# Optimization experiments

Measured on AMD Instinct MI355X. Metric: run time of the kernel, lower is better.

The kernel has to match this reference:

```python
import jax, jax.numpy as jnp
import numpy as np

NUM_CLASSES = 13
MIN_PTS = 50
CLUSTER_THRESHOLD = 0.3
MAX_CLUSTERS = 10
PROB_THRESH = 0.05


def _fps_indices(pts, valid, S):
    # Deterministic farthest-point sampling restricted to `valid` points.
    # Invalid points get min-distance -inf so they are never selected.
    neg = jnp.where(valid, 0.0, -jnp.inf)  # [N]
    start = jnp.argmax(valid)  # first valid point

    def d2_to(i):
        return jnp.sum((pts - pts[i]) ** 2, axis=-1)  # [N]

    mind = d2_to(start) + neg

    def step(mind, _):
        nxt = jnp.argmax(mind)
        mind = jnp.minimum(mind, d2_to(nxt) + neg)
        return mind, nxt

    _, rest = jax.lax.scan(step, mind, None, length=S - 1)
    return jnp.concatenate([start[None], rest])  # [S]


def _per_class(shifted, prob):
    # shifted: [N,3] shifted coords; prob: [N] softmax prob of this class.
    valid = prob > PROB_THRESH
    count = jnp.sum(valid)
    # num_seeds = min(max_clusters, count // min_pts, count); seeds k >= num_seeds are masked out
    num_seeds = jnp.minimum(jnp.minimum(MAX_CLUSTERS, count // MIN_PTS), count)
    idx = _fps_indices(shifted, valid, MAX_CLUSTERS)
    seeds = shifted[idx]  # [S,3]
    d2 = jnp.sum((shifted[:, None, :] - seeds[None, :, :]) ** 2, axis=-1)  # [N,S]
    sigma = CLUSTER_THRESHOLD * 0.5
    w = jnp.exp(-d2 / (2.0 * sigma * sigma))  # Gaussian soft ball query
    seed_valid = jnp.arange(MAX_CLUSTERS) < num_seeds  # [S]
    w = w * seed_valid[None, :].astype(w.dtype)
    assign = w / (jnp.sum(w, axis=-1, keepdims=True) + 1e-8)  # soft assignment over seeds
    # scatter into full mask == multiply by class prob gated by threshold membership
    final = assign * (prob * valid.astype(prob.dtype))[:, None]  # [N,S]
    return final.T, seed_valid  # [S,N], [S]


def _forward(semantic_logits, points, offsets):
    probs = jax.nn.softmax(semantic_logits, axis=-1)  # [B,N,C]
    shifted = points + offsets  # [B,N,3]
    per_class_all = jax.vmap(_per_class, in_axes=(None, 1))  # map over classes

    def per_batch(sh, pr):
        masks, seed_valid = per_class_all(sh, pr)  # [C,S,N], [C,S]
        K = NUM_CLASSES * MAX_CLUSTERS
        masks = masks.reshape(K, -1)  # [K,N]
        sv = seed_valid.reshape(K)
        # softmax(mask*10) over instance axis, restricted to valid instance rows
        logits = jnp.where(sv[:, None], masks * 10.0, -jnp.inf)
        out = jax.nn.softmax(logits, axis=0)
        return jnp.where(sv[:, None], out, 0.0)

    return jax.vmap(per_batch)(shifted, probs)  # [B, C*S, N]


def setup_inputs() -> dict:
    key = jax.random.key(0)
    k1, k2, k3 = jax.random.split(key, 3)
    B, N, C = 2, 65536, NUM_CLASSES
    semantic_logits = jax.random.normal(k1, (B, N, C), dtype=jnp.float32)
    points = jax.random.uniform(k2, (B, N, 3), dtype=jnp.float32)  # unit cube
    offsets = jax.random.normal(k3, (B, N, 3), dtype=jnp.float32) * 0.05  # small predicted shifts
    return {"semantic_logits": semantic_logits, "points": points, "offsets": offsets}


def reference(semantic_logits, points, offsets):
    return _forward(semantic_logits, points, offsets)
```

## Files before the change

### kernel.cpp

```cpp
#include <hip/hip_runtime.h>
#include <cstdint>

#define NCLS 13
#define SMAX 10
#define PTHRESH 0.05f
#define FPS_SEG 8
#define FPS_T 512
#define FPS_PPT 16
#define NSLOT 8
#define BCPAD 32
#define GABLK 256
#define BB 2
#define SLOT_DWORDS (BB * NCLS * SMAX * NSLOT * 2)

__device__ __forceinline__ float d2f(float ax, float ay, float az,
                                     float bx, float by, float bz) {
    float dx = ax - bx;
    float dy = ay - by;
    float dz = az - bz;
    return __fadd_rn(__fadd_rn(__fmul_rn(dx, dx), __fmul_rn(dy, dy)), __fmul_rn(dz, dz));
}

__device__ __forceinline__ unsigned int fmono(float f) {
    unsigned int u = __float_as_uint(f);
    return (u & 0x80000000u) ? ~u : (u | 0x80000000u);
}

__global__ void k_setup(const float* __restrict__ logits, const float* __restrict__ pts,
                        const float* __restrict__ offs, float* __restrict__ probs,
                        float4* __restrict__ xyzw, unsigned short* __restrict__ vmask,
                        unsigned int* __restrict__ pcnt, unsigned int* __restrict__ pfst,
                        unsigned int* __restrict__ slots32, int N) {
    int b = blockIdx.y;
    int n = blockIdx.x * blockDim.x + threadIdx.x;
    int t = threadIdx.x;
    __shared__ unsigned int sC[NCLS], sF[NCLS];
    if (t < NCLS) { sC[t] = 0u; sF[t] = 0xFFFFFFFFu; }
    __syncthreads();

    if (b == 0) {
        for (unsigned int i = blockIdx.x * blockDim.x + t; i < SLOT_DWORDS;
             i += GABLK * 256)
            slots32[i] = 0u;
    }

    if (n < N) {
        size_t bn = (size_t)b * N + n;
        const float* L = logits + bn * NCLS;
        float v[NCLS];
        float mx = -INFINITY;
#pragma unroll
        for (int c = 0; c < NCLS; ++c) { v[c] = L[c]; mx = fmaxf(mx, v[c]); }
        float s = 0.f;
#pragma unroll
        for (int c = 0; c < NCLS; ++c) { v[c] = expf(v[c] - mx); s += v[c]; }
        int lane = t & 63;
        int wave_base = n - lane;
        unsigned int msk = 0;
#pragma unroll
        for (int c = 0; c < NCLS; ++c) {
            float p = v[c] / s;
            probs[((size_t)b * NCLS + c) * N + n] = p;
            bool valid = p > PTHRESH;
            if (valid) msk |= (1u << c);
            unsigned long long m = __ballot(valid);
            if (lane == 0 && m) {
                atomicAdd(&sC[c], (unsigned int)__popcll(m));
                atomicMin(&sF[c], (unsigned int)(wave_base + __ffsll(m) - 1));
            }
        }
        float x = pts[bn * 3 + 0] + offs[bn * 3 + 0];
        float y = pts[bn * 3 + 1] + offs[bn * 3 + 1];
        float z = pts[bn * 3 + 2] + offs[bn * 3 + 2];
        xyzw[bn] = make_float4(x, y, z, 0.f);
        vmask[bn] = (unsigned short)msk;
    }
    __syncthreads();
    if (t < NCLS) {
        pcnt[(b * NCLS + t) * GABLK + blockIdx.x] = sC[t];
        pfst[(b * NCLS + t) * GABLK + blockIdx.x] = sF[t];
    }
}

__global__ __launch_bounds__(FPS_T, 1) void k_fps(
    const float4* __restrict__ xyzw, const unsigned short* __restrict__ vmask,
    const unsigned int* __restrict__ pcnt, const unsigned int* __restrict__ pfst,
    int* __restrict__ nseeds, float* __restrict__ seedxyz,
    unsigned long long* __restrict__ slots, int N) {
    int bid = blockIdx.x;
    int bc = bid & (BCPAD - 1);
    int g = bid >> 5;
    if (bc >= BB * NCLS) return;
    int b = bc / NCLS;
    int c = bc - b * NCLS;
    int t = threadIdx.x, lane = t & 63, w = t >> 6;

    const unsigned int* pc = pcnt + (size_t)bc * GABLK;
    const unsigned int* pf = pfst + (size_t)bc * GABLK;
    uint4 c4 = *(const uint4*)(pc + lane * 4);
    uint4 f4 = *(const uint4*)(pf + lane * 4);
    unsigned int cnt = c4.x + c4.y + c4.z + c4.w;
    unsigned int fst = min(min(f4.x, f4.y), min(f4.z, f4.w));
#pragma unroll
    for (int off = 1; off < 64; off <<= 1) {
        cnt += __shfl_xor(cnt, off, 64);
        fst = min(fst, __shfl_xor(fst, off, 64));
    }
    int ns = min(SMAX, min((int)cnt / 50, (int)cnt));
    if (g == 0 && t == 0) nseeds[bc] = ns;
    if (ns == 0) return;

    const float4* P4 = xyzw + (size_t)b * N;
    const unsigned short* VM = vmask + (size_t)b * N;

    int base = g * (FPS_T * FPS_PPT) + t;
    float X[FPS_PPT], Y[FPS_PPT], Z[FPS_PPT], m[FPS_PPT];
    unsigned int vm = 0;
#pragma unroll
    for (int j = 0; j < FPS_PPT; ++j) {
        int n = base + (j << 9);
        float4 q = P4[n];
        X[j] = q.x; Y[j] = q.y; Z[j] = q.z;
        if ((VM[n] >> c) & 1) vm |= (1u << j);
        m[j] = INFINITY;
    }

    int st = (int)fst;
    float4 q0 = P4[st];
    float cx = q0.x, cy = q0.y, cz = q0.z;
    if (g == 0 && t == 0) {
        float* sd = seedxyz + (size_t)bc * SMAX * 3;
        sd[0] = cx; sd[1] = cy; sd[2] = cz;
    }

    __shared__ unsigned long long s_keys[2][FPS_T / 64];

    for (int s = 1; s < ns; ++s) {
        float best = -INFINITY;
        int bidx = 0;
#pragma unroll
        for (int j = 0; j < FPS_PPT; ++j) {
            int n = base + (j << 9);
            float d2 = d2f(X[j], Y[j], Z[j], cx, cy, cz);
            float add = ((vm >> j) & 1u) ? 0.0f : -INFINITY;
            float nm = fminf(m[j], __fadd_rn(d2, add));
            m[j] = nm;
            if (nm > best) { best = nm; bidx = n; }
        }
        unsigned long long key =
            ((unsigned long long)fmono(best) << 32) | (unsigned int)(~(unsigned int)bidx);
#pragma unroll
        for (int off = 1; off < 64; off <<= 1) {
            unsigned long long ok = __shfl_xor(key, off, 64);
            if (ok > key) key = ok;
        }
        int par = s & 1;
        if (lane == 0) s_keys[par][w] = key;
        __syncthreads();

        unsigned long long* sl = slots + ((size_t)bc * SMAX + s) * NSLOT;
        if (w == 0) {
            unsigned long long bk = (lane < 8) ? s_keys[par][lane] : 0ULL;
#pragma unroll
            for (int off = 1; off < 8; off <<= 1) {
                unsigned long long ok = __shfl_xor(bk, off, 8);
                if (ok > bk) bk = ok;
            }
            if (lane == 0)
                __hip_atomic_store(&sl[g], bk, __ATOMIC_RELAXED, __HIP_MEMORY_SCOPE_AGENT);
        }
        asm volatile("" ::: "memory");
        unsigned long long kk = 0ULL;
        while (true) {
            if (lane < NSLOT && kk == 0ULL)
                kk = __hip_atomic_load(&sl[lane], __ATOMIC_RELAXED,
                                       __HIP_MEMORY_SCOPE_AGENT);
            if (__all(kk != 0ULL || lane >= NSLOT)) break;
        }
        asm volatile("" ::: "memory");
#pragma unroll
        for (int off = 1; off < 8; off <<= 1) {
            unsigned long long ok = __shfl_xor(kk, off, 8);
            if (ok > kk) kk = ok;
        }
        kk = __shfl(kk, 0, 64);

        int widx = (int)(~(unsigned int)kk);
        float4 qw = P4[widx];
        cx = qw.x; cy = qw.y; cz = qw.z;
        if (g == 0 && t == 0) {
            float* sd = seedxyz + ((size_t)bc * SMAX + s) * 3;
            sd[0] = cx; sd[1] = cy; sd[2] = cz;
        }
    }
}

__global__ __launch_bounds__(512) void k_out(
    const float* __restrict__ probs, const float4* __restrict__ xyzw,
    const int* __restrict__ nseeds, const float* __restrict__ seedxyz,
    float* __restrict__ out, int N) {
    int b = blockIdx.y;
    int t = threadIdx.x;
    int lane = t & 63;
    int wv = t >> 6;
    int n0 = blockIdx.x * 128 + lane * 2;

    __shared__ float S[NCLS * SMAX * 3];
    __shared__ int NSs[NCLS];
    __shared__ float gdS[NCLS][128];
    __shared__ float psum[8][128];
    if (t < NCLS * SMAX * 3) S[t] = seedxyz[(size_t)b * NCLS * SMAX * 3 + t];
    if (t >= 448 && t < 448 + NCLS) NSs[t - 448] = nseeds[b * NCLS + (t - 448)];
    __syncthreads();

    float4 q0 = xyzw[(size_t)b * N + n0];
    float4 q1 = xyzw[(size_t)b * N + n0 + 1];

    const float kinv = 22.2222222f;
    float ps0 = 0.f, ps1 = 0.f;
#pragma unroll
    for (int c = wv; c < NCLS; c += 8) {
        int ns = NSs[c];
        float gdv0 = 0.f, gdv1 = 0.f;
        if (ns > 0) {
            float2 pv = *(const float2*)(probs + ((size_t)b * NCLS + c) * N + n0);
            if (pv.x > PTHRESH) {
                float wb[SMAX]; float sw = 0.f;
#pragma unroll
                for (int s = 0; s < SMAX; ++s) {
                    wb[s] = 0.f;
                    if (s < ns) {
                        const float* sd = &S[(c * SMAX + s) * 3];
                        float d2 = d2f(q0.x, q0.y, q0.z, sd[0], sd[1], sd[2]);
                        wb[s] = __expf(-d2 * kinv);
                        sw += wb[s];
                    }
                }
                gdv0 = __fdividef(pv.x, sw + 1e-8f);
#pragma unroll
                for (int s = 0; s < SMAX; ++s)
                    if (s < ns) ps0 += __expf(10.f * wb[s] * gdv0);
            } else {
                ps0 += (float)ns;
            }
            if (pv.y > PTHRESH) {
                float wb[SMAX]; float sw = 0.f;
#pragma unroll
                for (int s = 0; s < SMAX; ++s) {
                    wb[s] = 0.f;
                    if (s < ns) {
                        const float* sd = &S[(c * SMAX + s) * 3];
                        float d2 = d2f(q1.x, q1.y, q1.z, sd[0], sd[1], sd[2]);
                        wb[s] = __expf(-d2 * kinv);
                        sw += wb[s];
                    }
                }
                gdv1 = __fdividef(pv.y, sw + 1e-8f);
#pragma unroll
                for (int s = 0; s < SMAX; ++s)
                    if (s < ns) ps1 += __expf(10.f * wb[s] * gdv1);
            } else {
                ps1 += (float)ns;
            }
        }
        gdS[c][lane * 2] = gdv0;
        gdS[c][lane * 2 + 1] = gdv1;
    }
    psum[wv][lane * 2] = ps0;
    psum[wv][lane * 2 + 1] = ps1;
    __syncthreads();

    float tot0 = 0.f, tot1 = 0.f;
#pragma unroll
    for (int w = 0; w < 8; ++w) {
        tot0 += psum[w][lane * 2];
        tot1 += psum[w][lane * 2 + 1];
    }
    float inv0 = __fdividef(1.f, tot0);
    float inv1 = __fdividef(1.f, tot1);

    float* ob = out + (size_t)b * (NCLS * SMAX) * N + n0;
#pragma unroll
    for (int k = 0; k < NCLS * SMAX; k += 8) {
        int kk = k + wv;
        if (kk >= NCLS * SMAX) break;
        int c = kk / SMAX, s = kk - c * SMAX;
        float o0 = 0.f, o1 = 0.f;
        if (s < NSs[c]) {
            float g0 = gdS[c][lane * 2];
            float g1 = gdS[c][lane * 2 + 1];
            const float* sd = &S[(c * SMAX + s) * 3];
            if (g0 > 0.f) {
                float d2 = d2f(q0.x, q0.y, q0.z, sd[0], sd[1], sd[2]);
                o0 = __expf(10.f * __expf(-d2 * kinv) * g0) * inv0;
            } else {
                o0 = inv0;
            }
            if (g1 > 0.f) {
                float d2 = d2f(q1.x, q1.y, q1.z, sd[0], sd[1], sd[2]);
                o1 = __expf(10.f * __expf(-d2 * kinv) * g1) * inv1;
            } else {
                o1 = inv1;
            }
        }
        float2 st; st.x = o0; st.y = o1;
        *(float2*)(ob + (size_t)kk * N) = st;
    }
}

extern "C" void kernel_launch(void* const* d_in, const int* in_sizes, int n_in,
                              void* d_out, int out_size, void* d_ws, size_t ws_size,
                              hipStream_t stream) {
    const float* logits = (const float*)d_in[0];
    const float* pts    = (const float*)d_in[1];
    const float* offs   = (const float*)d_in[2];
    float* out = (float*)d_out;

    const int B = BB;
    const int BN = in_sizes[0] / NCLS;
    const int N = BN / B;

    char* w = (char*)d_ws;
    size_t off = 0;
    auto take = [&](size_t bytes) -> void* {
        void* p = w + off;
        off = (off + bytes + 255) & ~(size_t)255;
        return p;
    };
    float* probs   = (float*)take((size_t)B * NCLS * N * sizeof(float));
    float4* xyzw   = (float4*)take((size_t)B * N * sizeof(float4));
    unsigned short* vmsk = (unsigned short*)take((size_t)B * N * sizeof(unsigned short));
    float* seedxyz = (float*)take((size_t)B * NCLS * SMAX * 3 * sizeof(float));
    unsigned int* pcnt = (unsigned int*)take((size_t)B * NCLS * GABLK * sizeof(unsigned int));
    unsigned int* pfst = (unsigned int*)take((size_t)B * NCLS * GABLK * sizeof(unsigned int));
    int* nseeds        = (int*)take(B * NCLS * sizeof(int));
    unsigned long long* slots =
        (unsigned long long*)take((size_t)B * NCLS * SMAX * NSLOT * sizeof(unsigned long long));

    dim3 gA((N + 255) / 256, B);
    k_setup<<<gA, 256, 0, stream>>>(logits, pts, offs, probs, xyzw, vmsk,
                                    pcnt, pfst, (unsigned int*)slots, N);

    k_fps<<<BCPAD * FPS_SEG, FPS_T, 0, stream>>>(xyzw, vmsk, pcnt, pfst,
                                                 nseeds, seedxyz, slots, N);

    dim3 gC(N / 128, B);
    k_out<<<gC, 512, 0, stream>>>(probs, xyzw, nseeds, seedxyz, out, N);
}
```

Before: 64.16 us.

## Cache per-seed exponentials in LDS and process one point per thread

The output kernel now stores each seed's softmax numerator in a shared-memory table during the first pass and reads it back in the write pass. Before, the distance and two exponentials were computed a second time there. Blocks shrink to 256 threads with one point per thread instead of two, and the grid doubles. The trade-off is about 33KB of LDS per block, which may limit occupancy, and output stores are now scalar rather than float2.

```diff
diff --git a/kernel.cpp b/kernel.cpp
--- a/kernel.cpp
+++ b/kernel.cpp
@@ -11,6 +11,7 @@
 #define BCPAD 32
 #define GABLK 256
 #define BB 2
+#define OUT_T 256
 #define SLOT_DWORDS (BB * NCLS * SMAX * NSLOT * 2)
 
 __device__ __forceinline__ float d2f(float ax, float ay, float az,
@@ -195,7 +196,7 @@
     }
 }
 
-__global__ __launch_bounds__(512) void k_out(
+__global__ __launch_bounds__(OUT_T) void k_out(
     const float* __restrict__ probs, const float4* __restrict__ xyzw,
     const int* __restrict__ nseeds, const float* __restrict__ seedxyz,
     float* __restrict__ out, int N) {
@@ -203,108 +204,69 @@
     int t = threadIdx.x;
     int lane = t & 63;
     int wv = t >> 6;
-    int n0 = blockIdx.x * 128 + lane * 2;
+    int n = blockIdx.x * 64 + lane;
 
     __shared__ float S[NCLS * SMAX * 3];
     __shared__ int NSs[NCLS];
-    __shared__ float gdS[NCLS][128];
-    __shared__ float psum[8][128];
-    if (t < NCLS * SMAX * 3) S[t] = seedxyz[(size_t)b * NCLS * SMAX * 3 + t];
-    if (t >= 448 && t < 448 + NCLS) NSs[t - 448] = nseeds[b * NCLS + (t - 448)];
+    __shared__ float gdS[NCLS][64];
+    __shared__ float psum[4][64];
+    __shared__ float E[NCLS * SMAX][64];
+    for (int i = t; i < NCLS * SMAX * 3; i += OUT_T)
+        S[i] = seedxyz[(size_t)b * NCLS * SMAX * 3 + i];
+    if (t < NCLS) NSs[t] = nseeds[b * NCLS + t];
     __syncthreads();
 
-    float4 q0 = xyzw[(size_t)b * N + n0];
-    float4 q1 = xyzw[(size_t)b * N + n0 + 1];
+    float4 q = xyzw[(size_t)b * N + n];
 
     const float kinv = 22.2222222f;
-    float ps0 = 0.f, ps1 = 0.f;
-#pragma unroll
-    for (int c = wv; c < NCLS; c += 8) {
+    float ps = 0.f;
+    for (int c = wv; c < NCLS; c += 4) {
         int ns = NSs[c];
-        float gdv0 = 0.f, gdv1 = 0.f;
+        float gdv = 0.f;
         if (ns > 0) {
-            float2 pv = *(const float2*)(probs + ((size_t)b * NCLS + c) * N + n0);
-            if (pv.x > PTHRESH) {
-                float wb[SMAX]; float sw = 0.f;
+            float pv = probs[((size_t)b * NCLS + c) * N + n];
+            if (pv > PTHRESH) {
+                float wb[SMAX];
+                float sw = 0.f;
 #pragma unroll
                 for (int s = 0; s < SMAX; ++s) {
                     wb[s] = 0.f;
                     if (s < ns) {
                         const float* sd = &S[(c * SMAX + s) * 3];
-                        float d2 = d2f(q0.x, q0.y, q0.z, sd[0], sd[1], sd[2]);
+                        float d2 = d2f(q.x, q.y, q.z, sd[0], sd[1], sd[2]);
                         wb[s] = __expf(-d2 * kinv);
                         sw += wb[s];
                     }
                 }
-                gdv0 = __fdividef(pv.x, sw + 1e-8f);
+                gdv = __fdividef(pv, sw + 1e-8f);
 #pragma unroll
                 for (int s = 0; s < SMAX; ++s)
-                    if (s < ns) ps0 += __expf(10.f * wb[s] * gdv0);
+                    if (s < ns) {
+                        float e = __expf(10.f * wb[s] * gdv);
+                        E[c * SMAX + s][lane] = e;
+                        ps += e;
+                    }
             } else {
-                ps0 += (float)ns;
+                ps += (float)ns;
             }
-            if (pv.y > PTHRESH) {
-                float wb[SMAX]; float sw = 0.f;
-#pragma unroll
-                for (int s = 0; s < SMAX; ++s) {
-                    wb[s] = 0.f;
-                    if (s < ns) {
-                        const float* sd = &S[(c * SMAX + s) * 3];
-                        float d2 = d2f(q1.x, q1.y, q1.z, sd[0], sd[1], sd[2]);
-                        wb[s] = __expf(-d2 * kinv);
-                        sw += wb[s];
-                    }
-                }
-                gdv1 = __fdividef(pv.y, sw + 1e-8f);
-#pragma unroll
-                for (int s = 0; s < SMAX; ++s)
-                    if (s < ns) ps1 += __expf(10.f * wb[s] * gdv1);
-            } else {
-                ps1 += (float)ns;
-            }
-        }
-        gdS[c][lane * 2] = gdv0;
-        gdS[c][lane * 2 + 1] = gdv1;
-    }
-    psum[wv][lane * 2] = ps0;
-    psum[wv][lane * 2 + 1] = ps1;
+        }
+        gdS[c][lane] = gdv;
+    }
+    psum[wv][lane] = ps;
     __syncthreads();
 
-    float tot0 = 0.f, tot1 = 0.f;
-#pragma unroll
-    for (int w = 0; w < 8; ++w) {
-        tot0 += psum[w][lane * 2];
-        tot1 += psum[w][lane * 2 + 1];
-    }
-    float inv0 = __fdividef(1.f, tot0);
-    float inv1 = __fdividef(1.f, tot1);
-
-    float* ob = out + (size_t)b * (NCLS * SMAX) * N + n0;
-#pragma unroll
-    for (int k = 0; k < NCLS * SMAX; k += 8) {
-        int kk = k + wv;
-        if (kk >= NCLS * SMAX) break;
+    float tot = psum[0][lane] + psum[1][lane] + psum[2][lane] + psum[3][lane];
+    float inv = __fdividef(1.f, tot);
+
+    float* ob = out + (size_t)b * (NCLS * SMAX) * N + n;
+    for (int kk = wv; kk < NCLS * SMAX; kk += 4) {
         int c = kk / SMAX, s = kk - c * SMAX;
-        float o0 = 0.f, o1 = 0.f;
+        float o = 0.f;
         if (s < NSs[c]) {
-            float g0 = gdS[c][lane * 2];
-            float g1 = gdS[c][lane * 2 + 1];
-            const float* sd = &S[(c * SMAX + s) * 3];
-            if (g0 > 0.f) {
-                float d2 = d2f(q0.x, q0.y, q0.z, sd[0], sd[1], sd[2]);
-                o0 = __expf(10.f * __expf(-d2 * kinv) * g0) * inv0;
-            } else {
-                o0 = inv0;
-            }
-            if (g1 > 0.f) {
-                float d2 = d2f(q1.x, q1.y, q1.z, sd[0], sd[1], sd[2]);
-                o1 = __expf(10.f * __expf(-d2 * kinv) * g1) * inv1;
-            } else {
-                o1 = inv1;
-            }
-        }
-        float2 st; st.x = o0; st.y = o1;
-        *(float2*)(ob + (size_t)kk * N) = st;
+            float gdv = gdS[c][lane];
+            o = (gdv > 0.f) ? E[kk][lane] * inv : inv;
+        }
+        ob[(size_t)kk * N] = o;
     }
 }
 
@@ -344,6 +306,6 @@
     k_fps<<<BCPAD * FPS_SEG, FPS_T, 0, stream>>>(xyzw, vmsk, pcnt, pfst,
                                                  nseeds, seedxyz, slots, N);
 
-    dim3 gC(N / 128, B);
-    k_out<<<gC, 512, 0, stream>>>(probs, xyzw, nseeds, seedxyz, out, N);
-}
+    dim3 gC(N / 64, B);
+    k_out<<<gC, OUT_T, 0, stream>>>(probs, xyzw, nseeds, seedxyz, out, N);
+}
```

Result: slower. 69.13 us (+7.7%).

## Recompute softmax in output kernel and cache exp terms in shared memory

Applied to the files above, without the earlier changes.

Stops writing the class-major probability buffer in the setup kernel. The output kernel now reloads the logits, recomputes the softmax per point, and uses the saved validity bitmask instead of a probability threshold test. It also stores every per-seed exponential in a large shared array, so the final write pass only scales by the inverse sum instead of recomputing distances and two exps. This cuts global traffic and duplicated transcendental work, but it raises shared memory use per block (about 66KB), which may lower occupancy, and it re-reads the logits through strided per-point loads.

```diff
diff --git a/kernel.cpp b/kernel.cpp
--- a/kernel.cpp
+++ b/kernel.cpp
@@ -11,6 +11,7 @@
 #define BCPAD 32
 #define GABLK 256
 #define BB 2
+#define OUT_T 512
 #define SLOT_DWORDS (BB * NCLS * SMAX * NSLOT * 2)
 
 __device__ __forceinline__ float d2f(float ax, float ay, float az,
@@ -27,7 +28,7 @@
 }
 
 __global__ void k_setup(const float* __restrict__ logits, const float* __restrict__ pts,
-                        const float* __restrict__ offs, float* __restrict__ probs,
+                        const float* __restrict__ offs,
                         float4* __restrict__ xyzw, unsigned short* __restrict__ vmask,
                         unsigned int* __restrict__ pcnt, unsigned int* __restrict__ pfst,
                         unsigned int* __restrict__ slots32, int N) {
@@ -60,7 +61,6 @@
 #pragma unroll
         for (int c = 0; c < NCLS; ++c) {
             float p = v[c] / s;
-            probs[((size_t)b * NCLS + c) * N + n] = p;
             bool valid = p > PTHRESH;
             if (valid) msk |= (1u << c);
             unsigned long long m = __ballot(valid);
@@ -195,8 +195,9 @@
     }
 }
 
-__global__ __launch_bounds__(512) void k_out(
-    const float* __restrict__ probs, const float4* __restrict__ xyzw,
+__global__ __launch_bounds__(OUT_T) void k_out(
+    const float* __restrict__ logits, const float4* __restrict__ xyzw,
+    const unsigned short* __restrict__ vmask,
     const int* __restrict__ nseeds, const float* __restrict__ seedxyz,
     float* __restrict__ out, int N) {
     int b = blockIdx.y;
@@ -204,107 +205,121 @@
     int lane = t & 63;
     int wv = t >> 6;
     int n0 = blockIdx.x * 128 + lane * 2;
+    int l2 = lane * 2;
 
     __shared__ float S[NCLS * SMAX * 3];
     __shared__ int NSs[NCLS];
-    __shared__ float gdS[NCLS][128];
     __shared__ float psum[8][128];
+    __shared__ float E[NCLS * SMAX][128];
     if (t < NCLS * SMAX * 3) S[t] = seedxyz[(size_t)b * NCLS * SMAX * 3 + t];
     if (t >= 448 && t < 448 + NCLS) NSs[t - 448] = nseeds[b * NCLS + (t - 448)];
     __syncthreads();
 
-    float4 q0 = xyzw[(size_t)b * N + n0];
-    float4 q1 = xyzw[(size_t)b * N + n0 + 1];
+    size_t bn0 = (size_t)b * N + n0;
+    float4 q0 = xyzw[bn0];
+    float4 q1 = xyzw[bn0 + 1];
+    unsigned int vm0 = vmask[bn0];
+    unsigned int vm1 = vmask[bn0 + 1];
+
+    const float* L0 = logits + bn0 * NCLS;
+    const float* L1 = L0 + NCLS;
+    float mx0 = -INFINITY, mx1 = -INFINITY;
+#pragma unroll
+    for (int c = 0; c < NCLS; ++c) {
+        mx0 = fmaxf(mx0, L0[c]);
+        mx1 = fmaxf(mx1, L1[c]);
+    }
+    float dn0 = 0.f, dn1 = 0.f;
+#pragma unroll
+    for (int c = 0; c < NCLS; ++c) {
+        dn0 += __expf(L0[c] - mx0);
+        dn1 += __expf(L1[c] - mx1);
+    }
+    float rd0 = __fdividef(1.f, dn0);
+    float rd1 = __fdividef(1.f, dn1);
 
     const float kinv = 22.2222222f;
     float ps0 = 0.f, ps1 = 0.f;
-#pragma unroll
     for (int c = wv; c < NCLS; c += 8) {
         int ns = NSs[c];
-        float gdv0 = 0.f, gdv1 = 0.f;
-        if (ns > 0) {
-            float2 pv = *(const float2*)(probs + ((size_t)b * NCLS + c) * N + n0);
-            if (pv.x > PTHRESH) {
-                float wb[SMAX]; float sw = 0.f;
-#pragma unroll
-                for (int s = 0; s < SMAX; ++s) {
-                    wb[s] = 0.f;
-                    if (s < ns) {
-                        const float* sd = &S[(c * SMAX + s) * 3];
-                        float d2 = d2f(q0.x, q0.y, q0.z, sd[0], sd[1], sd[2]);
-                        wb[s] = __expf(-d2 * kinv);
-                        sw += wb[s];
-                    }
+        if (ns == 0) continue;
+        if ((vm0 >> c) & 1) {
+            float pv = __expf(L0[c] - mx0) * rd0;
+            float wb[SMAX]; float sw = 0.f;
+#pragma unroll
+            for (int s = 0; s < SMAX; ++s) {
+                wb[s] = 0.f;
+                if (s < ns) {
+                    const float* sd = &S[(c * SMAX + s) * 3];
+                    float d2 = d2f(q0.x, q0.y, q0.z, sd[0], sd[1], sd[2]);
+                    wb[s] = __expf(-d2 * kinv);
+                    sw += wb[s];
                 }
-                gdv0 = __fdividef(pv.x, sw + 1e-8f);
-#pragma unroll
-                for (int s = 0; s < SMAX; ++s)
-                    if (s < ns) ps0 += __expf(10.f * wb[s] * gdv0);
-            } else {
-                ps0 += (float)ns;
             }
-            if (pv.y > PTHRESH) {
-                float wb[SMAX]; float sw = 0.f;
-#pragma unroll
-                for (int s = 0; s < SMAX; ++s) {
-                    wb[s] = 0.f;
-                    if (s < ns) {
-                        const float* sd = &S[(c * SMAX + s) * 3];
-                        float d2 = d2f(q1.x, q1.y, q1.z, sd[0], sd[1], sd[2]);
-                        wb[s] = __expf(-d2 * kinv);
-                        sw += wb[s];
-                    }
+            float gd = __fdividef(pv, sw + 1e-8f);
+#pragma unroll
+            for (int s = 0; s < SMAX; ++s)
+                if (s < ns) {
+                    float e = __expf(10.f * wb[s] * gd);
+                    E[c * SMAX + s][l2] = e;
+                    ps0 += e;
                 }
-                gdv1 = __fdividef(pv.y, sw + 1e-8f);
-#pragma unroll
-                for (int s = 0; s < SMAX; ++s)
-                    if (s < ns) ps1 += __expf(10.f * wb[s] * gdv1);
-            } else {
-                ps1 += (float)ns;
+        } else {
+#pragma unroll
+            for (int s = 0; s < SMAX; ++s)
+                if (s < ns) E[c * SMAX + s][l2] = 1.0f;
+            ps0 += (float)ns;
+        }
+        if ((vm1 >> c) & 1) {
+            float pv = __expf(L1[c] - mx1) * rd1;
+            float wb[SMAX]; float sw = 0.f;
+#pragma unroll
+            for (int s = 0; s < SMAX; ++s) {
+                wb[s] = 0.f;
+                if (s < ns) {
+                    const float* sd = &S[(c * SMAX + s) * 3];
+                    float d2 = d2f(q1.x, q1.y, q1.z, sd[0], sd[1], sd[2]);
+                    wb[s] = __expf(-d2 * kinv);
+                    sw += wb[s];
+                }
             }
-        }
-        gdS[c][lane * 2] = gdv0;
-        gdS[c][lane * 2 + 1] = gdv1;
-    }
-    psum[wv][lane * 2] = ps0;
-    psum[wv][lane * 2 + 1] = ps1;
+            float gd = __fdividef(pv, sw + 1e-8f);
+#pragma unroll
+            for (int s = 0; s < SMAX; ++s)
+                if (s < ns) {
+                    float e = __expf(10.f * wb[s] * gd);
+                    E[c * SMAX + s][l2 + 1] = e;
+                    ps1 += e;
+                }
+        } else {
+#pragma unroll
+            for (int s = 0; s < SMAX; ++s)
+                if (s < ns) E[c * SMAX + s][l2 + 1] = 1.0f;
+            ps1 += (float)ns;
+        }
+    }
+    psum[wv][l2] = ps0;
+    psum[wv][l2 + 1] = ps1;
     __syncthreads();
 
     float tot0 = 0.f, tot1 = 0.f;
 #pragma unroll
     for (int w = 0; w < 8; ++w) {
-        tot0 += psum[w][lane * 2];
-        tot1 += psum[w][lane * 2 + 1];
+        tot0 += psum[w][l2];
+        tot1 += psum[w][l2 + 1];
     }
     float inv0 = __fdividef(1.f, tot0);
     float inv1 = __fdividef(1.f, tot1);
 
     float* ob = out + (size_t)b * (NCLS * SMAX) * N + n0;
-#pragma unroll
-    for (int k = 0; k < NCLS * SMAX; k += 8) {
-        int kk = k + wv;
-        if (kk >= NCLS * SMAX) break;
+    for (int kk = wv; kk < NCLS * SMAX; kk += 8) {
         int c = kk / SMAX, s = kk - c * SMAX;
-        float o0 = 0.f, o1 = 0.f;
+        float2 o; o.x = 0.f; o.y = 0.f;
         if (s < NSs[c]) {
-            float g0 = gdS[c][lane * 2];
-            float g1 = gdS[c][lane * 2 + 1];
-            const float* sd = &S[(c * SMAX + s) * 3];
-            if (g0 > 0.f) {
-                float d2 = d2f(q0.x, q0.y, q0.z, sd[0], sd[1], sd[2]);
-                o0 = __expf(10.f * __expf(-d2 * kinv) * g0) * inv0;
-            } else {
-                o0 = inv0;
-            }
-            if (g1 > 0.f) {
-                float d2 = d2f(q1.x, q1.y, q1.z, sd[0], sd[1], sd[2]);
-                o1 = __expf(10.f * __expf(-d2 * kinv) * g1) * inv1;
-            } else {
-                o1 = inv1;
-            }
-        }
-        float2 st; st.x = o0; st.y = o1;
-        *(float2*)(ob + (size_t)kk * N) = st;
+            o.x = E[kk][l2] * inv0;
+            o.y = E[kk][l2 + 1] * inv1;
+        }
+        *(float2*)(ob + (size_t)kk * N) = o;
     }
 }
 
@@ -327,7 +342,6 @@
         off = (off + bytes + 255) & ~(size_t)255;
         return p;
     };
-    float* probs   = (float*)take((size_t)B * NCLS * N * sizeof(float));
     float4* xyzw   = (float4*)take((size_t)B * N * sizeof(float4));
     unsigned short* vmsk = (unsigned short*)take((size_t)B * N * sizeof(unsigned short));
     float* seedxyz = (float*)take((size_t)B * NCLS * SMAX * 3 * sizeof(float));
@@ -338,12 +352,12 @@
         (unsigned long long*)take((size_t)B * NCLS * SMAX * NSLOT * sizeof(unsigned long long));
 
     dim3 gA((N + 255) / 256, B);
-    k_setup<<<gA, 256, 0, stream>>>(logits, pts, offs, probs, xyzw, vmsk,
+    k_setup<<<gA, 256, 0, stream>>>(logits, pts, offs, xyzw, vmsk,
                                     pcnt, pfst, (unsigned int*)slots, N);
 
     k_fps<<<BCPAD * FPS_SEG, FPS_T, 0, stream>>>(xyzw, vmsk, pcnt, pfst,
                                                  nseeds, seedxyz, slots, N);
 
     dim3 gC(N / 128, B);
-    k_out<<<gC, 512, 0, stream>>>(probs, xyzw, nseeds, seedxyz, out, N);
-}
+    k_out<<<gC, OUT_T, 0, stream>>>(logits, xyzw, vmsk, nseeds, seedxyz, out, N);
+}
```

Measured after the change: 64.37 us. No clear change (+0.3%).
